# Optimization experiments

Hardware: AMD Instinct MI355X
Metric: run time of the kernel (lower is better)

Reference implementation:

```python
import jax, jax.numpy as jnp
import numpy as np

LAYER_NORM_EPS = 1e-6
N_HEAD, D_MODEL, D_HEAD = 16, 1024, 64
QLEN, RLEN, BSZ = 2048, 2048, 2


def _rel_shift(x):
    # x: [T, C, b, n] -> Transformer-XL relative shift
    T, C = x.shape[0], x.shape[1]
    tail = x.shape[2:]
    zero_pad = jnp.zeros((T, 1) + tail, dtype=x.dtype)
    x_padded = jnp.concatenate([zero_pad, x], axis=1)          # [T, C+1, b, n]
    x_padded = x_padded.reshape((C + 1, T) + tail)             # [C+1, T, b, n]
    return x_padded[1:].reshape(x.shape)                       # [T, C, b, n]


def _layer_norm(x, gamma, beta):
    mu = jnp.mean(x, axis=-1, keepdims=True)
    var = jnp.mean(jnp.square(x - mu), axis=-1, keepdims=True)
    return (x - mu) * jax.lax.rsqrt(var + LAYER_NORM_EPS) * gamma + beta


def setup_inputs() -> dict:
    key = jax.random.key(0)
    ks = jax.random.split(key, 8)
    s_qkv = 1.0 / np.sqrt(D_MODEL)
    return {
        "h": jax.random.normal(ks[0], (QLEN, BSZ, D_MODEL), jnp.float32),
        "r": jax.random.normal(ks[1], (RLEN, D_MODEL), jnp.float32),
        "r_w_bias": jax.random.normal(ks[2], (N_HEAD, D_HEAD), jnp.float32) * 0.02,
        "r_r_bias": jax.random.normal(ks[3], (N_HEAD, D_HEAD), jnp.float32) * 0.02,
        "W_qkv": jax.random.normal(ks[4], (D_MODEL, 3 * N_HEAD * D_HEAD), jnp.float32) * s_qkv,
        "W_r": jax.random.normal(ks[5], (D_MODEL, N_HEAD * D_HEAD), jnp.float32) * s_qkv,
        "W_o": jax.random.normal(ks[6], (N_HEAD * D_HEAD, D_MODEL), jnp.float32) * s_qkv,
        "ln_gamma": jnp.ones((D_MODEL,), jnp.float32),
        "ln_beta": jnp.zeros((D_MODEL,), jnp.float32),
    }


def reference(h, r, r_w_bias, r_r_bias, W_qkv, W_r, W_o, ln_gamma, ln_beta):
    qlen, bsz = h.shape[0], h.shape[1]
    n_head, d_head = N_HEAD, D_HEAD
    scale = 1.0 / np.sqrt(d_head).astype(np.float32)

    w_heads = h @ W_qkv                                   # [q, b, 3*n*d]
    w_q, w_k, w_v = jnp.split(w_heads, 3, axis=-1)
    r_k = (r @ W_r).reshape(r.shape[0], n_head, d_head)    # [rlen, n, d]

    klen = w_k.shape[0]
    w_q = w_q.reshape(qlen, bsz, n_head, d_head)
    w_k = w_k.reshape(klen, bsz, n_head, d_head)
    w_v = w_v.reshape(klen, bsz, n_head, d_head)

    AC = jnp.einsum('ibnd,jbnd->ijbn', w_q + r_w_bias, w_k)
    BD = jnp.einsum('ibnd,jnd->ijbn', w_q + r_r_bias, r_k)
    BD = _rel_shift(BD)

    attn_score = (AC + BD) * scale                         # [q, k, b, n]
    attn_prob = jax.nn.softmax(attn_score, axis=1)

    attn_vec = jnp.einsum('ijbn,jbnd->ibnd', attn_prob, w_v)
    attn_vec = attn_vec.reshape(qlen, bsz, n_head * d_head)
    attn_out = attn_vec @ W_o                              # [q, b, d_model]

    # post-norm residual (pre_norm=False)
    return _layer_norm(h + attn_out, ln_gamma, ln_beta)
```

## Files before the change

kernel.cpp:

```cpp
#include <hip/hip_runtime.h>
#include <hip/hip_bf16.h>

typedef unsigned short u16;
typedef __attribute__((ext_vector_type(8))) short s16x8;
typedef __attribute__((ext_vector_type(8))) unsigned short u16x8;
typedef __attribute__((ext_vector_type(4))) float f32x4;

#define SEQ 2048
#define KEXP 0.18033688011112042f

__device__ __forceinline__ float bf2f(u16 x) {
  union { unsigned u; float f; } c; c.u = ((unsigned)x) << 16; return c.f;
}
__device__ __forceinline__ u16 f2bf(float f) {
  __hip_bfloat16 h = __float2bfloat16(f);
  return __builtin_bit_cast(u16, h);
}
__device__ __forceinline__ unsigned pack2(float a, float b) {
  return (unsigned)f2bf(a) | ((unsigned)f2bf(b) << 16);
}

__global__ __launch_bounds__(256) void k_cvt(const float* __restrict__ src,
                                             u16* __restrict__ dst, int n4) {
  int i = blockIdx.x * 256 + threadIdx.x;
  if (i >= n4) return;
  float4 v = ((const float4*)src)[i];
  ((ushort4*)dst)[i] = make_ushort4(f2bf(v.x), f2bf(v.y), f2bf(v.z), f2bf(v.w));
}

__global__ __launch_bounds__(256) void k_tcvt(const float* __restrict__ src,
                                              u16* __restrict__ dst, int R, int C) {
  __shared__ u16 T[64][72];
  int r0 = blockIdx.y * 64, c0 = blockIdx.x * 64;
  int tid = threadIdx.x;
#pragma unroll
  for (int p = 0; p < 4; ++p) {
    int f = p * 256 + tid;
    int r = f >> 4, cc = (f & 15) * 4;
    float4 v = *(const float4*)(src + (size_t)(r0 + r) * C + c0 + cc);
    T[r][cc + 0] = f2bf(v.x); T[r][cc + 1] = f2bf(v.y);
    T[r][cc + 2] = f2bf(v.z); T[r][cc + 3] = f2bf(v.w);
  }
  __syncthreads();
#pragma unroll
  for (int p = 0; p < 2; ++p) {
    int f = p * 256 + tid;
    int c = f >> 3, rr = (f & 7) * 8;
    u16x8 v;
#pragma unroll
    for (int e = 0; e < 8; ++e) v[e] = T[rr + e][c];
    *(u16x8*)(dst + (size_t)(c0 + c) * R + r0 + rr) = v;
  }
}

template <int RES>
__global__ __launch_bounds__(256) void k_gemm_bt(const u16* __restrict__ A,
                                                 const u16* __restrict__ Bt,
                                                 u16* __restrict__ Cb,
                                                 float* __restrict__ Cf,
                                                 const float* __restrict__ res,
                                                 int M, int N, int K) {
  __shared__ u16 As[128 * 72];
  __shared__ u16 Bs[128 * 72];
  const int tid = threadIdx.x;
  const int l = tid & 63, wv = tid >> 6;
  const int g = l >> 4, c16 = l & 15;
  const int m0 = blockIdx.x * 128, n0 = blockIdx.y * 128;
  const int wr = (wv >> 1) * 64, wc = (wv & 1) * 64;
  f32x4 acc[4][4] = {};
  for (int k0 = 0; k0 < K; k0 += 64) {
    __syncthreads();
#pragma unroll
    for (int p = 0; p < 4; ++p) {
      int f = p * 256 + tid;
      int row = f >> 3, kb = (f & 7) * 8;
      u16x8 va = *(const u16x8*)(A + (size_t)(m0 + row) * K + k0 + kb);
      u16x8 vb = *(const u16x8*)(Bt + (size_t)(n0 + row) * K + k0 + kb);
      *(u16x8*)&As[row * 72 + kb] = va;
      *(u16x8*)&Bs[row * 72 + kb] = vb;
    }
    __syncthreads();
#pragma unroll
    for (int ks = 0; ks < 2; ++ks) {
      s16x8 af[4], bf[4];
#pragma unroll
      for (int fr = 0; fr < 4; ++fr)
        af[fr] = *(const s16x8*)&As[(wr + fr * 16 + c16) * 72 + ks * 32 + g * 8];
#pragma unroll
      for (int fc = 0; fc < 4; ++fc)
        bf[fc] = *(const s16x8*)&Bs[(wc + fc * 16 + c16) * 72 + ks * 32 + g * 8];
#pragma unroll
      for (int fr = 0; fr < 4; ++fr)
#pragma unroll
        for (int fc = 0; fc < 4; ++fc)
          acc[fr][fc] = __builtin_amdgcn_mfma_f32_16x16x32_bf16(af[fr], bf[fc],
                                                                acc[fr][fc], 0, 0, 0);
    }
  }
#pragma unroll
  for (int fr = 0; fr < 4; ++fr)
#pragma unroll
    for (int fc = 0; fc < 4; ++fc)
#pragma unroll
      for (int reg = 0; reg < 4; ++reg) {
        int row = m0 + wr + fr * 16 + g * 4 + reg;
        int col = n0 + wc + fc * 16 + c16;
        float v = acc[fr][fc][reg];
        if (RES) Cf[(size_t)row * N + col] = v + res[(size_t)row * N + col];
        else     Cb[(size_t)row * N + col] = f2bf(v);
      }
}

__global__ __launch_bounds__(256) void k_vt(const u16* __restrict__ qkv,
                                            u16* __restrict__ vT) {
  __shared__ u16 T[64][72];
  const int tid = threadIdx.x;
  const int j0 = blockIdx.x * 64;
  const int n = blockIdx.y & 15, b = blockIdx.y >> 4;
#pragma unroll
  for (int p = 0; p < 2; ++p) {
    int f = p * 256 + tid;
    int r = f >> 3, cc = (f & 7) * 8;
    *(u16x8*)&T[r][cc] =
        *(const u16x8*)(qkv + ((size_t)((j0 + r) * 2 + b)) * 3072 + 2048 + n * 64 + cc);
  }
  __syncthreads();
#pragma unroll
  for (int p = 0; p < 2; ++p) {
    int f = p * 256 + tid;
    int d = f >> 3, jc = (f & 7) * 8;
    u16x8 v;
#pragma unroll
    for (int e = 0; e < 8; ++e) v[e] = T[jc + e][d];
    *(u16x8*)(vT + ((size_t)((b * 16 + n) * 64 + d)) * 2048 + j0 + jc) = v;
  }
}

__global__ __launch_bounds__(256) void k_attn(const u16* __restrict__ qkv,
                                              const u16* __restrict__ rk,
                                              const u16* __restrict__ vT,
                                              const float* __restrict__ rwb,
                                              const float* __restrict__ rrb,
                                              u16* __restrict__ av) {
  __shared__ u16 Kt[128][72];
  __shared__ u16 Vt[64][136];
  __shared__ u16 St2[65 * 200];
  __shared__ u16 Pt[4][16][136];

  const int tid = threadIdx.x;
  const int l = tid & 63, wv = tid >> 6;
  const int g = l >> 4, c16 = l & 15;
  const int s = blockIdx.x;
  const int y = (s & 7) + 8 * (s >> 8);
  const int x = (s >> 3) & 31;
  const int i0 = x * 64;
  const int n = y & 15, b = y >> 4;
  const int ii = wv * 16 + c16;
  const f32x4 zero4 = {0.f, 0.f, 0.f, 0.f};
  const s16x8 zero8 = {0, 0, 0, 0, 0, 0, 0, 0};

  s16x8 qw[2];
  {
    int i = i0 + wv * 16 + c16;
    const u16* src = qkv + ((size_t)(i * 2 + b)) * 3072 + n * 64;
#pragma unroll
    for (int ks = 0; ks < 2; ++ks) {
      int d0 = ks * 32 + g * 8;
      u16x8 raw = *(const u16x8*)(src + d0);
      u16x8 wq;
#pragma unroll
      for (int e = 0; e < 8; ++e)
        wq[e] = f2bf(bf2f(raw[e]) + rwb[n * 64 + d0 + e]);
      qw[ks] = __builtin_bit_cast(s16x8, wq);
    }
  }
  s16x8 qr_b[4][2];
#pragma unroll
  for (int rb = 0; rb < 4; ++rb) {
    int i = i0 + rb * 16 + c16;
    const u16* src = qkv + ((size_t)(i * 2 + b)) * 3072 + n * 64;
#pragma unroll
    for (int ks = 0; ks < 2; ++ks) {
      int d0 = ks * 32 + g * 8;
      u16x8 raw = *(const u16x8*)(src + d0);
      u16x8 wq;
#pragma unroll
      for (int e = 0; e < 8; ++e)
        wq[e] = f2bf(bf2f(raw[e]) + rrb[n * 64 + d0 + e]);
      qr_b[rb][ks] = __builtin_bit_cast(s16x8, wq);
    }
  }
  s16x8 q64[2];
  {
    int i = i0 + 64; if (i > SEQ - 1) i = SEQ - 1;
    const u16* src = qkv + ((size_t)(i * 2 + b)) * 3072 + n * 64;
#pragma unroll
    for (int ks = 0; ks < 2; ++ks) {
      int d0 = ks * 32 + g * 8;
      u16x8 raw = *(const u16x8*)(src + d0);
      u16x8 wq;
#pragma unroll
      for (int e = 0; e < 8; ++e)
        wq[e] = f2bf(bf2f(raw[e]) + rrb[n * 64 + d0 + e]);
      q64[ks] = __builtin_bit_cast(s16x8, wq);
    }
  }

  u16x8 kpre[4], vpre[4];
  s16x8 rpre[3][2];
  auto issue_loads = [&](int j0n) {
#pragma unroll
    for (int p = 0; p < 4; ++p) {
      int f = p * 256 + tid;
      kpre[p] = *(const u16x8*)(qkv + ((size_t)((j0n + (f >> 3)) * 2 + b)) * 3072 +
                                1024 + n * 64 + (f & 7) * 8);
    }
#pragma unroll
    for (int p = 0; p < 4; ++p) {
      int f = p * 256 + tid;
      vpre[p] = *(const u16x8*)(vT + ((size_t)((b * 16 + n) * 64 + (f >> 4))) * 2048 +
                                j0n + (f & 15) * 8);
    }
#pragma unroll
    for (int c3 = 0; c3 < 3; ++c3) {
      int w = (wv * 3 + c3) * 16 + c16;
      int u = j0n - i0 - 63 + w;
      int c = (u <= 0) ? (u + (SEQ - 1)) : (u - 2);
      const u16* p = rk + (size_t)(c < 0 ? 0 : c) * 1024 + n * 64;
      rpre[c3][0] = *(const s16x8*)(p + g * 8);
      rpre[c3][1] = *(const s16x8*)(p + 32 + g * 8);
      if (c < 0) { rpre[c3][0] = zero8; rpre[c3][1] = zero8; }
    }
  };

  float m_prev = -1e30f, l_sum = 0.f;
  f32x4 o_acc[4];
#pragma unroll
  for (int r = 0; r < 4; ++r) o_acc[r] = zero4;

  issue_loads(0);

  for (int it = 0; it < 16; ++it) {
    const int j0 = it * 128;
    const int wbthr = (64 + i0 - j0) >> 4;
    __syncthreads();

#pragma unroll
    for (int p = 0; p < 4; ++p) {
      int f = p * 256 + tid;
      *(u16x8*)&Kt[f >> 3][(f & 7) * 8] = kpre[p];
    }
#pragma unroll
    for (int p = 0; p < 4; ++p) {
      int f = p * 256 + tid;
      *(u16x8*)&Vt[f >> 4][(f & 15) * 8] = vpre[p];
    }

#pragma unroll
    for (int c3 = 0; c3 < 3; ++c3) {
      const int wb = wv * 3 + c3;
      const int du = (wb >= wbthr) ? 1 : 0;
#pragma unroll
      for (int rb = 0; rb < 4; ++rb) {
        f32x4 q = zero4;
        q = __builtin_amdgcn_mfma_f32_16x16x32_bf16(rpre[c3][0], qr_b[rb][0], q, 0, 0, 0);
        q = __builtin_amdgcn_mfma_f32_16x16x32_bf16(rpre[c3][1], qr_b[rb][1], q, 0, 0, 0);
        uint2 pk;
        pk.x = pack2(q[0], q[1]);
        pk.y = pack2(q[2], q[3]);
        *(uint2*)&St2[(rb * 16 + c16 + 1 - du) * 200 + wb * 16 + g * 4] = pk;
      }
      {
        f32x4 q = zero4;
        q = __builtin_amdgcn_mfma_f32_16x16x32_bf16(rpre[c3][0], q64[0], q, 0, 0, 0);
        q = __builtin_amdgcn_mfma_f32_16x16x32_bf16(rpre[c3][1], q64[1], q, 0, 0, 0);
        if (du && c16 == 0) {
          uint2 pk;
          pk.x = pack2(q[0], q[1]);
          pk.y = pack2(q[2], q[3]);
          *(uint2*)&St2[64 * 200 + wb * 16 + g * 4] = pk;
        }
      }
    }
    __syncthreads();

    f32x4 sc[8];
#pragma unroll
    for (int fj = 0; fj < 8; ++fj) sc[fj] = zero4;
#pragma unroll
    for (int ks = 0; ks < 2; ++ks)
#pragma unroll
      for (int fj = 0; fj < 8; ++fj) {
        s16x8 kf = *(const s16x8*)&Kt[fj * 16 + c16][ks * 32 + g * 8];
        sc[fj] = __builtin_amdgcn_mfma_f32_16x16x32_bf16(kf, qw[ks], sc[fj], 0, 0, 0);
      }

    {
      const u16* Sb = &St2[ii * 199 + 263 + g * 4];
#pragma unroll
      for (int fj = 0; fj < 8; ++fj)
#pragma unroll
        for (int reg = 0; reg < 4; ++reg)
          sc[fj][reg] += bf2f(Sb[fj * 16 + reg]);
    }

    float mt = sc[0][0];
#pragma unroll
    for (int fj = 0; fj < 8; ++fj)
#pragma unroll
      for (int reg = 0; reg < 4; ++reg)
        mt = fmaxf(mt, sc[fj][reg]);
    mt = fmaxf(mt, __shfl_xor(mt, 16));
    mt = fmaxf(mt, __shfl_xor(mt, 32));
    float mn = fmaxf(m_prev, mt);
    float al = __builtin_amdgcn_exp2f((m_prev - mn) * KEXP);
    m_prev = mn;
    float mk = mn * KEXP;
    float rs = 0.f;
#pragma unroll
    for (int fj = 0; fj < 8; ++fj)
#pragma unroll
      for (int reg = 0; reg < 4; ++reg) {
        float p = __builtin_amdgcn_exp2f(fmaf(sc[fj][reg], KEXP, -mk));
        rs += p;
        sc[fj][reg] = p;
      }
    rs += __shfl_xor(rs, 16);
    rs += __shfl_xor(rs, 32);
    l_sum = l_sum * al + rs;

    float al_t[4];
#pragma unroll
    for (int reg = 0; reg < 4; ++reg)
      al_t[reg] = __shfl(al, g * 4 + reg, 64);
#pragma unroll
    for (int fd = 0; fd < 4; ++fd)
#pragma unroll
      for (int reg = 0; reg < 4; ++reg)
        o_acc[fd][reg] *= al_t[reg];

#pragma unroll
    for (int fj = 0; fj < 8; ++fj) {
      uint2 pk;
      pk.x = pack2(sc[fj][0], sc[fj][1]);
      pk.y = pack2(sc[fj][2], sc[fj][3]);
      *(uint2*)&Pt[wv][c16][fj * 16 + g * 4] = pk;
    }

    if (it < 15) issue_loads(j0 + 128);

#pragma unroll
    for (int ks = 0; ks < 4; ++ks) {
      s16x8 pa = *(const s16x8*)&Pt[wv][c16][ks * 32 + g * 8];
#pragma unroll
      for (int fd = 0; fd < 4; ++fd) {
        s16x8 vb = *(const s16x8*)&Vt[fd * 16 + c16][ks * 32 + g * 8];
        o_acc[fd] = __builtin_amdgcn_mfma_f32_16x16x32_bf16(pa, vb, o_acc[fd], 0, 0, 0);
      }
    }
  }

  float linv = 1.0f / l_sum;
  float linv_t[4];
#pragma unroll
  for (int reg = 0; reg < 4; ++reg)
    linv_t[reg] = __shfl(linv, g * 4 + reg, 64);
#pragma unroll
  for (int reg = 0; reg < 4; ++reg) {
    int i = i0 + wv * 16 + g * 4 + reg;
    u16* dst = av + ((size_t)(i * 2 + b)) * 1024 + n * 64;
#pragma unroll
    for (int fd = 0; fd < 4; ++fd)
      dst[fd * 16 + c16] = f2bf(o_acc[fd][reg] * linv_t[reg]);
  }
}

__global__ __launch_bounds__(256) void k_ln(const float* __restrict__ tmp,
                                            const float* __restrict__ gamma,
                                            const float* __restrict__ beta,
                                            float* __restrict__ out) {
  __shared__ float r1[4], r2[4];
  const int row = blockIdx.x, tid = threadIdx.x;
  const float* x = tmp + (size_t)row * 1024;
  float4 v = *(const float4*)(x + tid * 4);
  float s1 = v.x + v.y + v.z + v.w;
  float s2 = v.x * v.x + v.y * v.y + v.z * v.z + v.w * v.w;
#pragma unroll
  for (int off = 1; off < 64; off <<= 1) {
    s1 += __shfl_xor(s1, off, 64);
    s2 += __shfl_xor(s2, off, 64);
  }
  if ((tid & 63) == 0) { r1[tid >> 6] = s1; r2[tid >> 6] = s2; }
  __syncthreads();
  s1 = r1[0] + r1[1] + r1[2] + r1[3];
  s2 = r2[0] + r2[1] + r2[2] + r2[3];
  float mu = s1 * (1.f / 1024.f);
  float var = s2 * (1.f / 1024.f) - mu * mu;
  float rstd = rsqrtf(var + 1e-6f);
  float4 gm = *(const float4*)(gamma + tid * 4);
  float4 bt = *(const float4*)(beta + tid * 4);
  float4 o;
  o.x = (v.x - mu) * rstd * gm.x + bt.x;
  o.y = (v.y - mu) * rstd * gm.y + bt.y;
  o.z = (v.z - mu) * rstd * gm.z + bt.z;
  o.w = (v.w - mu) * rstd * gm.w + bt.w;
  *(float4*)(out + (size_t)row * 1024 + tid * 4) = o;
}

extern "C" void kernel_launch(void* const* d_in, const int* in_sizes, int n_in,
                              void* d_out, int out_size, void* d_ws, size_t ws_size,
                              hipStream_t stream) {
  const float* h    = (const float*)d_in[0];
  const float* r    = (const float*)d_in[1];
  const float* rwb  = (const float*)d_in[2];
  const float* rrb  = (const float*)d_in[3];
  const float* Wqkv = (const float*)d_in[4];
  const float* Wr   = (const float*)d_in[5];
  const float* Wo   = (const float*)d_in[6];
  const float* gam  = (const float*)d_in[7];
  const float* bet  = (const float*)d_in[8];
  float* out = (float*)d_out;

  u16* hb     = (u16*)d_ws;
  u16* Wqkv_t = hb + (size_t)4096 * 1024;
  u16* Wr_t   = Wqkv_t + (size_t)3072 * 1024;
  u16* Wo_t   = Wr_t + (size_t)1024 * 1024;
  u16* rb     = Wo_t + (size_t)1024 * 1024;
  u16* qkv    = rb + (size_t)2048 * 1024;
  u16* rk     = qkv + (size_t)4096 * 3072;
  u16* vT     = rk + (size_t)2048 * 1024;
  u16* av     = vT + (size_t)2 * 16 * 64 * 2048;
  float* tmp  = (float*)(av + (size_t)4096 * 1024);

  k_cvt<<<4096, 256, 0, stream>>>(h, hb, 4096 * 1024 / 4);
  k_cvt<<<2048, 256, 0, stream>>>(r, rb, 2048 * 1024 / 4);
  k_tcvt<<<dim3(48, 16), 256, 0, stream>>>(Wqkv, Wqkv_t, 1024, 3072);
  k_tcvt<<<dim3(16, 16), 256, 0, stream>>>(Wr, Wr_t, 1024, 1024);
  k_tcvt<<<dim3(16, 16), 256, 0, stream>>>(Wo, Wo_t, 1024, 1024);
  k_gemm_bt<0><<<dim3(32, 24), 256, 0, stream>>>(hb, Wqkv_t, qkv, nullptr, nullptr,
                                                 4096, 3072, 1024);
  k_gemm_bt<0><<<dim3(16, 8), 256, 0, stream>>>(rb, Wr_t, rk, nullptr, nullptr,
                                                2048, 1024, 1024);
  k_vt<<<dim3(32, 32), 256, 0, stream>>>(qkv, vT);
  k_attn<<<1024, 256, 0, stream>>>(qkv, rk, vT, rwb, rrb, av);
  k_gemm_bt<1><<<dim3(32, 8), 256, 0, stream>>>(av, Wo_t, nullptr, tmp, h,
                                                4096, 1024, 1024);
  k_ln<<<4096, 256, 0, stream>>>(tmp, gam, bet, out);
}
```

Baseline: 279.2 us.

## Add lazy softmax rescaling, prefetch bias gathers, and MFMA priority hints

The attention inner loop now only updates the running max and rescales the output accumulator when some lane's new max exceeds the old one by a threshold (FA4-style lazy rescale), skipping the shuffle and multiply on most iterations. The rel-shift bias reads from shared memory are split and issued around the QK MFMAs to hide LDS latency. s_setprio raises wave priority around the MFMA blocks, and the max and sum reductions use four independent chains for more ILP. The lazy rescale lets exponentials grow up to 2^(44*KEXP) before rescaling, which risks precision loss or overflow if score ranges are large.

```diff
diff --git a/kernel.cpp b/kernel.cpp
--- a/kernel.cpp
+++ b/kernel.cpp
@@ -206,6 +206,8 @@
     }
   }
 
+  const u16* Sb = &St2[ii * 199 + 263 + g * 4];
+
   u16x8 kpre[4], vpre[4];
   s16x8 rpre[3][2];
   auto issue_loads = [&](int j0n) {
@@ -284,9 +286,17 @@
     }
     __syncthreads();
 
+    u16 gta[16];
+#pragma unroll
+    for (int fj = 0; fj < 4; ++fj)
+#pragma unroll
+      for (int reg = 0; reg < 4; ++reg)
+        gta[fj * 4 + reg] = Sb[fj * 16 + reg];
+
     f32x4 sc[8];
 #pragma unroll
     for (int fj = 0; fj < 8; ++fj) sc[fj] = zero4;
+    __builtin_amdgcn_s_setprio(1);
 #pragma unroll
     for (int ks = 0; ks < 2; ++ks)
 #pragma unroll
@@ -294,50 +304,67 @@
         s16x8 kf = *(const s16x8*)&Kt[fj * 16 + c16][ks * 32 + g * 8];
         sc[fj] = __builtin_amdgcn_mfma_f32_16x16x32_bf16(kf, qw[ks], sc[fj], 0, 0, 0);
       }
-
-    {
-      const u16* Sb = &St2[ii * 199 + 263 + g * 4];
-#pragma unroll
-      for (int fj = 0; fj < 8; ++fj)
-#pragma unroll
-        for (int reg = 0; reg < 4; ++reg)
-          sc[fj][reg] += bf2f(Sb[fj * 16 + reg]);
-    }
-
-    float mt = sc[0][0];
-#pragma unroll
-    for (int fj = 0; fj < 8; ++fj)
+    __builtin_amdgcn_s_setprio(0);
+
+    u16 gtb[16];
+#pragma unroll
+    for (int fj = 0; fj < 4; ++fj)
 #pragma unroll
       for (int reg = 0; reg < 4; ++reg)
-        mt = fmaxf(mt, sc[fj][reg]);
+        gtb[fj * 4 + reg] = Sb[(fj + 4) * 16 + reg];
+#pragma unroll
+    for (int fj = 0; fj < 4; ++fj)
+#pragma unroll
+      for (int reg = 0; reg < 4; ++reg) {
+        sc[fj][reg] += bf2f(gta[fj * 4 + reg]);
+        sc[fj + 4][reg] += bf2f(gtb[fj * 4 + reg]);
+      }
+
+    float m0 = sc[0][0], m1 = sc[0][1], m2 = sc[0][2], m3 = sc[0][3];
+#pragma unroll
+    for (int fj = 1; fj < 8; ++fj) {
+      m0 = fmaxf(m0, sc[fj][0]); m1 = fmaxf(m1, sc[fj][1]);
+      m2 = fmaxf(m2, sc[fj][2]); m3 = fmaxf(m3, sc[fj][3]);
+    }
+    float mt = fmaxf(fmaxf(m0, m1), fmaxf(m2, m3));
     mt = fmaxf(mt, __shfl_xor(mt, 16));
     mt = fmaxf(mt, __shfl_xor(mt, 32));
-    float mn = fmaxf(m_prev, mt);
-    float al = __builtin_amdgcn_exp2f((m_prev - mn) * KEXP);
-    m_prev = mn;
-    float mk = mn * KEXP;
-    float rs = 0.f;
-#pragma unroll
-    for (int fj = 0; fj < 8; ++fj)
-#pragma unroll
-      for (int reg = 0; reg < 4; ++reg) {
-        float p = __builtin_amdgcn_exp2f(fmaf(sc[fj][reg], KEXP, -mk));
-        rs += p;
-        sc[fj][reg] = p;
-      }
+
+    const int need = __any(mt - m_prev > 44.0f);
+    float al = 1.0f;
+    if (need) {
+      float mn = fmaxf(m_prev, mt);
+      al = __builtin_amdgcn_exp2f((m_prev - mn) * KEXP);
+      m_prev = mn;
+    }
+    const float mk = m_prev * KEXP;
+
+    float r0 = 0.f, r1 = 0.f, r2 = 0.f, r3 = 0.f;
+#pragma unroll
+    for (int fj = 0; fj < 8; ++fj) {
+      float p0 = __builtin_amdgcn_exp2f(fmaf(sc[fj][0], KEXP, -mk));
+      float p1 = __builtin_amdgcn_exp2f(fmaf(sc[fj][1], KEXP, -mk));
+      float p2 = __builtin_amdgcn_exp2f(fmaf(sc[fj][2], KEXP, -mk));
+      float p3 = __builtin_amdgcn_exp2f(fmaf(sc[fj][3], KEXP, -mk));
+      r0 += p0; r1 += p1; r2 += p2; r3 += p3;
+      sc[fj][0] = p0; sc[fj][1] = p1; sc[fj][2] = p2; sc[fj][3] = p3;
+    }
+    float rs = (r0 + r1) + (r2 + r3);
     rs += __shfl_xor(rs, 16);
     rs += __shfl_xor(rs, 32);
-    l_sum = l_sum * al + rs;
-
-    float al_t[4];
-#pragma unroll
-    for (int reg = 0; reg < 4; ++reg)
-      al_t[reg] = __shfl(al, g * 4 + reg, 64);
-#pragma unroll
-    for (int fd = 0; fd < 4; ++fd)
+    l_sum = fmaf(l_sum, al, rs);
+
+    if (need) {
+      float al_t[4];
 #pragma unroll
       for (int reg = 0; reg < 4; ++reg)
-        o_acc[fd][reg] *= al_t[reg];
+        al_t[reg] = __shfl(al, g * 4 + reg, 64);
+#pragma unroll
+      for (int fd = 0; fd < 4; ++fd)
+#pragma unroll
+        for (int reg = 0; reg < 4; ++reg)
+          o_acc[fd][reg] *= al_t[reg];
+    }
 
 #pragma unroll
     for (int fj = 0; fj < 8; ++fj) {
@@ -349,6 +376,7 @@
 
     if (it < 15) issue_loads(j0 + 128);
 
+    __builtin_amdgcn_s_setprio(1);
 #pragma unroll
     for (int ks = 0; ks < 4; ++ks) {
       s16x8 pa = *(const s16x8*)&Pt[wv][c16][ks * 32 + g * 8];
@@ -358,6 +386,7 @@
         o_acc[fd] = __builtin_amdgcn_mfma_f32_16x16x32_bf16(pa, vb, o_acc[fd], 0, 0, 0);
       }
     }
+    __builtin_amdgcn_s_setprio(0);
   }
 
   float linv = 1.0f / l_sum;
```

Result: slower. 286.2 us (+2.5%).
